# Optimization experiments

Hardware: AMD Instinct MI355X
Metric: run time of the kernel (lower is better)

The kernel has to match this reference:

```python
import jax, jax.numpy as jnp
import numpy as np

NUM_VARS = 10000
NUM_CLAUSES = 100000
K = 3  # literals per clause (3-SAT)
BATCH = 256


def setup_inputs() -> dict:
    key = jax.random.key(0)
    k1, k2, k3 = jax.random.split(key, 3)
    # fuzzy truth assignments in [0,1): [num_vars, batch]
    input = jax.random.uniform(k1, (NUM_VARS, BATCH), dtype=jnp.float32)
    # clause-literal incidence: variable index and negation flag per slot
    lit_idx = jax.random.randint(k2, (NUM_CLAUSES, K), 0, NUM_VARS, dtype=jnp.int64)
    lit_neg = jax.random.randint(k3, (NUM_CLAUSES, K), 0, 2, dtype=jnp.int64)
    return {"input": input, "lit_idx": lit_idx, "lit_neg": lit_neg}


def reference(input, lit_idx, lit_neg):
    # Gather literal values per clause slot: [num_clauses, K, batch]
    vals = input[lit_idx]
    # Goedel negation for negated literals: x -> 1 - x
    vals = jnp.where((lit_neg == 1)[:, :, None], 1.0 - vals, vals)
    # Fuzzy disjunction (Goedel = max) within each clause: [num_clauses, batch]
    clause_vals = jnp.max(vals, axis=1)
    # Fuzzy conjunction (Goedel = min) across clauses: [batch]
    return jnp.min(clause_vals, axis=0)
```

## Files before the change

### kernel.cpp

```cpp
#include <hip/hip_runtime.h>
#include <hip/hip_fp16.h>

#define NUM_VARS    10000
#define NUM_CLAUSES 100000
#define BATCH       256

typedef __attribute__((ext_vector_type(4))) _Float16 half4_t;
typedef __attribute__((ext_vector_type(4))) float    float4_t;

__global__ __launch_bounds__(256) void fuzzy_convert_init(
    const float4_t* __restrict__ in,
    half4_t*        __restrict__ out16,
    float*          __restrict__ out)
{
    if (blockIdx.x == 0 && threadIdx.x < BATCH)
        out[threadIdx.x] = __uint_as_float(0x7F800000u);

    const int n4 = NUM_VARS * BATCH / 4;
    for (int i = blockIdx.x * blockDim.x + threadIdx.x; i < n4;
         i += gridDim.x * blockDim.x) {
        float4_t v = in[i];
        half4_t h;
        h.x = (_Float16)v.x;
        h.y = (_Float16)v.y;
        h.z = (_Float16)v.z;
        h.w = (_Float16)v.w;
        out16[i] = h;
    }
}

__global__ __launch_bounds__(512, 4) void fuzzy_cnf_kernel(
    const half4_t* __restrict__ input16,
    const int*     __restrict__ lit_idx,
    const int*     __restrict__ lit_neg,
    float*         __restrict__ out)
{
    const int wave        = threadIdx.x >> 6;
    const int lane        = threadIdx.x & 63;
    const int gwave       = blockIdx.x * 8 + wave;
    const int total_waves = gridDim.x * 8;

    float4 acc = make_float4(1e30f, 1e30f, 1e30f, 1e30f);

    #pragma unroll 4
    for (int c = gwave; c < NUM_CLAUSES; c += total_waves) {
        const int base = c * 3;
        const int i0 = __builtin_amdgcn_readfirstlane(lit_idx[base + 0]);
        const int i1 = __builtin_amdgcn_readfirstlane(lit_idx[base + 1]);
        const int i2 = __builtin_amdgcn_readfirstlane(lit_idx[base + 2]);
        const float n0 = (float)__builtin_amdgcn_readfirstlane(lit_neg[base + 0]);
        const float n1 = (float)__builtin_amdgcn_readfirstlane(lit_neg[base + 1]);
        const float n2 = (float)__builtin_amdgcn_readfirstlane(lit_neg[base + 2]);

        const half4_t h0 = input16[i0 * 64 + lane];
        const half4_t h1 = input16[i1 * 64 + lane];
        const half4_t h2 = input16[i2 * 64 + lane];

        float4 m;
        m.x = fmaxf(fmaxf(fabsf((float)h0.x - n0), fabsf((float)h1.x - n1)), fabsf((float)h2.x - n2));
        m.y = fmaxf(fmaxf(fabsf((float)h0.y - n0), fabsf((float)h1.y - n1)), fabsf((float)h2.y - n2));
        m.z = fmaxf(fmaxf(fabsf((float)h0.z - n0), fabsf((float)h1.z - n1)), fabsf((float)h2.z - n2));
        m.w = fmaxf(fmaxf(fabsf((float)h0.w - n0), fabsf((float)h1.w - n1)), fabsf((float)h2.w - n2));

        acc.x = fminf(acc.x, m.x);
        acc.y = fminf(acc.y, m.y);
        acc.z = fminf(acc.z, m.z);
        acc.w = fminf(acc.w, m.w);
    }

    __shared__ float sm[8][BATCH];
    const int b0 = lane * 4;
    sm[wave][b0 + 0] = acc.x;
    sm[wave][b0 + 1] = acc.y;
    sm[wave][b0 + 2] = acc.z;
    sm[wave][b0 + 3] = acc.w;
    __syncthreads();

    const int t = threadIdx.x;
    if (t < BATCH) {
        float m = sm[0][t];
        #pragma unroll
        for (int w = 1; w < 8; ++w) m = fminf(m, sm[w][t]);
        atomicMin((unsigned int*)out + t, __float_as_uint(m));
    }
}

extern "C" void kernel_launch(void* const* d_in, const int* in_sizes, int n_in,
                              void* d_out, int out_size, void* d_ws, size_t ws_size,
                              hipStream_t stream) {
    const float* input   = (const float*)d_in[0];
    const int*   lit_idx = (const int*)d_in[1];
    const int*   lit_neg = (const int*)d_in[2];
    float*       out     = (float*)d_out;

    half4_t* input16 = (half4_t*)d_ws;

    fuzzy_convert_init<<<512, 256, 0, stream>>>((const float4_t*)input, input16, out);
    fuzzy_cnf_kernel<<<512, 512, 0, stream>>>(input16, lit_idx, lit_neg, out);
}
```

Before: 93.30 us.

## Split batch columns across XCD halves so each XCD caches half the input

Blocks are mapped by XCD index (blockIdx & 7) so that XCDs 0-3 handle batch columns 0-127 and XCDs 4-7 handle columns 128-255. Each wave now loads half2 per lane instead of half4, and the grid is doubled to keep the clause work per wave the same. The aim is to halve the working set of the fp16 input that each XCD's L2 must hold, which should improve L2 hit rates for the random gathers. In exchange, each clause's indices are read and broadcast twice, and the code relies on round-robin block-to-XCD assignment.

Result: faster. 90.97 us (-2.5%).

```diff
diff --git a/kernel.cpp b/kernel.cpp
--- a/kernel.cpp
+++ b/kernel.cpp
@@ -6,6 +6,7 @@
 #define BATCH       256
 
 typedef __attribute__((ext_vector_type(4))) _Float16 half4_t;
+typedef __attribute__((ext_vector_type(2))) _Float16 half2_t;
 typedef __attribute__((ext_vector_type(4))) float    float4_t;
 
 __global__ __launch_bounds__(256) void fuzzy_convert_init(
@@ -30,17 +31,21 @@
 }
 
 __global__ __launch_bounds__(512, 4) void fuzzy_cnf_kernel(
-    const half4_t* __restrict__ input16,
+    const half2_t* __restrict__ input16,
     const int*     __restrict__ lit_idx,
     const int*     __restrict__ lit_neg,
     float*         __restrict__ out)
 {
-    const int wave        = threadIdx.x >> 6;
-    const int lane        = threadIdx.x & 63;
-    const int gwave       = blockIdx.x * 8 + wave;
-    const int total_waves = gridDim.x * 8;
+    const int wave = threadIdx.x >> 6;
+    const int lane = threadIdx.x & 63;
+    const int xcd  = blockIdx.x & 7;
+    const int half = (xcd >= 4) ? 1 : 0;
+    const int halfBlock   = ((blockIdx.x >> 3) << 2) | (xcd & 3);
+    const int gwave       = halfBlock * 8 + wave;
+    const int total_waves = 4096;
+    const int colBase     = half * 64;
 
-    float4 acc = make_float4(1e30f, 1e30f, 1e30f, 1e30f);
+    float2 acc = make_float2(1e30f, 1e30f);
 
     #pragma unroll 4
     for (int c = gwave; c < NUM_CLAUSES; c += total_waves) {
@@ -52,36 +57,29 @@
         const float n1 = (float)__builtin_amdgcn_readfirstlane(lit_neg[base + 1]);
         const float n2 = (float)__builtin_amdgcn_readfirstlane(lit_neg[base + 2]);
 
-        const half4_t h0 = input16[i0 * 64 + lane];
-        const half4_t h1 = input16[i1 * 64 + lane];
-        const half4_t h2 = input16[i2 * 64 + lane];
+        const half2_t h0 = input16[i0 * 128 + colBase + lane];
+        const half2_t h1 = input16[i1 * 128 + colBase + lane];
+        const half2_t h2 = input16[i2 * 128 + colBase + lane];
 
-        float4 m;
+        float2 m;
         m.x = fmaxf(fmaxf(fabsf((float)h0.x - n0), fabsf((float)h1.x - n1)), fabsf((float)h2.x - n2));
         m.y = fmaxf(fmaxf(fabsf((float)h0.y - n0), fabsf((float)h1.y - n1)), fabsf((float)h2.y - n2));
-        m.z = fmaxf(fmaxf(fabsf((float)h0.z - n0), fabsf((float)h1.z - n1)), fabsf((float)h2.z - n2));
-        m.w = fmaxf(fmaxf(fabsf((float)h0.w - n0), fabsf((float)h1.w - n1)), fabsf((float)h2.w - n2));
 
         acc.x = fminf(acc.x, m.x);
         acc.y = fminf(acc.y, m.y);
-        acc.z = fminf(acc.z, m.z);
-        acc.w = fminf(acc.w, m.w);
     }
 
-    __shared__ float sm[8][BATCH];
-    const int b0 = lane * 4;
-    sm[wave][b0 + 0] = acc.x;
-    sm[wave][b0 + 1] = acc.y;
-    sm[wave][b0 + 2] = acc.z;
-    sm[wave][b0 + 3] = acc.w;
+    __shared__ float sm[8][128];
+    sm[wave][lane * 2 + 0] = acc.x;
+    sm[wave][lane * 2 + 1] = acc.y;
     __syncthreads();
 
     const int t = threadIdx.x;
-    if (t < BATCH) {
+    if (t < 128) {
         float m = sm[0][t];
         #pragma unroll
         for (int w = 1; w < 8; ++w) m = fminf(m, sm[w][t]);
-        atomicMin((unsigned int*)out + t, __float_as_uint(m));
+        atomicMin((unsigned int*)out + half * 128 + t, __float_as_uint(m));
     }
 }
 
@@ -95,6 +93,6 @@
 
     half4_t* input16 = (half4_t*)d_ws;
 
-    fuzzy_convert_init<<<512, 256, 0, stream>>>((const float4_t*)input, input16, out);
-    fuzzy_cnf_kernel<<<512, 512, 0, stream>>>(input16, lit_idx, lit_neg, out);
+    fuzzy_convert_init<<<1024, 256, 0, stream>>>((const float4_t*)input, input16, out);
+    fuzzy_cnf_kernel<<<1024, 512, 0, stream>>>((const half2_t*)input16, lit_idx, lit_neg, out);
 }
```
